# Kernel optimization log

Hardware: AMD Instinct MI355X
Metric: run time of the kernel (lower is better)

The kernel has to match this reference:

```python
import jax, jax.numpy as jnp
import numpy as np

B, IMSIZE, D, L, M, H = 8, 128, 64, 1, 16384, 100
N = B * IMSIZE * IMSIZE


def _build_edges(size, length):
    # build_perception: each pixel connects to all pixels within Chebyshev radius `length`
    ii, jj = np.meshgrid(np.arange(size), np.arange(size), indexing='ij')
    src, dst = [], []
    for dx in range(-length, length + 1):
        for dy in range(-length, length + 1):
            ok = (ii + dx >= 0) & (ii + dx < size) & (jj + dy >= 0) & (jj + dy < size)
            src.append((ii * size + jj)[ok])
            dst.append(((ii + dx) * size + (jj + dy))[ok])
    return np.concatenate(src), np.concatenate(dst)


def setup_inputs() -> dict:
    key = jax.random.key(0)
    ks = jax.random.split(key, 12)
    x = jax.random.normal(ks[0], (N, D), jnp.float32)  # RDN pixel features, flattened
    cluster = jax.random.randint(ks[1], (N,), 0, M).astype(jnp.int32)  # affinity-pool assignment
    s, d = _build_edges(IMSIZE, L)
    offs = (np.arange(B) * IMSIZE * IMSIZE)[:, None]
    edge_src = jnp.asarray((s[None] + offs).reshape(-1), jnp.int32)
    edge_dst = jnp.asarray((d[None] + offs).reshape(-1), jnp.int32)
    ii, jj = np.meshgrid(np.arange(IMSIZE), np.arange(IMSIZE), indexing='ij')
    g = np.stack([ii, jj], -1).reshape(-1, 2).astype(np.float32) / IMSIZE
    coords = jnp.asarray(np.tile(g, (B, 1)))  # spatial_coords.repeat(batch, 1)
    init = lambda k, sh: jax.random.normal(k, sh, jnp.float32) * 0.05
    params = dict(
        W1=init(ks[2], (D + 4, H)), b1=jnp.zeros((H,), jnp.float32),
        W2=init(ks[3], (H, H)), b2=jnp.zeros((H,), jnp.float32),
        W3=init(ks[4], (H, D)), b3=jnp.zeros((D,), jnp.float32),
        Wr=init(ks[5], (D, D)), Wn=init(ks[6], (D, D)), bg=jnp.zeros((D,), jnp.float32),
        Q1w=init(ks[7], (D, H)), Q1b=jnp.zeros((H,), jnp.float32),
        Q2w=init(ks[8], (H, H)), Q2b=jnp.zeros((H,), jnp.float32),
        Q3w=init(ks[9], (H, H)), Q3b=jnp.zeros((H,), jnp.float32),
        Q4w=init(ks[10], (H, 18)), Q4b=jnp.zeros((18,), jnp.float32),
    )
    out = dict(x=x, coords=coords, cluster=cluster, edge_src=edge_src, edge_dst=edge_dst)
    out.update(params)
    return out


def _render_qtr(G, feats):
    # RenderQTR, vectorized over the 3 channels: quadratic texture rendering per pixel
    centers, paras = feats[:, :2], feats[:, 2:20].reshape(-1, 3, 6)
    dx = (G[:, 0] - centers[:, 0])[:, None]
    dy = (G[:, 1] - centers[:, 1])[:, None]
    a, ah, aw, ahh, aww, ahw = (paras[:, :, k] for k in range(6))
    return a + ah * dx + aw * dy + ahh * dx * dx + aww * dy * dy + ahw * dx * dy


def reference(x, coords, cluster, edge_src, edge_dst, W1, b1, W2, b2, W3, b3, Wr, Wn, bg, Q1w, Q1b, Q2w, Q2b, Q3w, Q3b, Q4w, Q4b):
    # --- affinity-aggregation pooling (scatter-mean coarsening) ---
    cnt = jnp.maximum(jax.ops.segment_sum(jnp.ones((N, 1), x.dtype), cluster, num_segments=M), 1.0)
    xp = jax.ops.segment_sum(x, cluster, num_segments=M) / cnt
    cent = jax.ops.segment_sum(coords, cluster, num_segments=M) / cnt          # scatter_mean centroids
    mom = jax.ops.segment_sum(coords * coords, cluster, num_segments=M) / cnt  # scatter_mean moments
    # --- node transform FCBlock on [feat, 10*centroid, 10*moment] ---
    h = jnp.concatenate([xp, 10.0 * cent, 10.0 * mom], axis=-1)
    h = jax.nn.relu(h @ W1 + b1)
    h = jax.nn.relu(h @ W2 + b2)
    h = h @ W3 + b3
    # --- GraphConv(aggr='max') on cluster-coarsened edges (index-chase) ---
    cs, cd = cluster[edge_src], cluster[edge_dst]
    agg = jax.ops.segment_max((h @ Wn)[cs], cd, num_segments=M)
    agg = jnp.where(jnp.isfinite(agg), agg, 0.0)  # empty segments -> 0
    feat = h @ Wr + agg + bg
    # --- node_to_qtr_p2 FCBlock -> joint spatial features ---
    q = jax.nn.relu(feat @ Q1w + Q1b)
    q = jax.nn.relu(q @ Q2w + Q2b)
    q = jax.nn.relu(q @ Q3w + Q3b)
    q = q @ Q4w + Q4b
    jsf = jnp.concatenate([q, cent], axis=-1)[cluster]  # un-pool gather back to pixel nodes
    recon = _render_qtr(coords, jsf)                     # [N, 3]
    return recon.reshape(B, IMSIZE * IMSIZE, 3)          # to_dense_batch (equal-size batches)
```

## Files before the change

### kernel.cpp

```cpp
#include <hip/hip_runtime.h>
#include <hip/hip_fp16.h>
#include <cmath>

#define SSZ    128
#define SS     (SSZ*SSZ)
#define NB     8
#define NNODES (NB*SS)
#define DD     64
#define MM     16384
#define HH     100
#define BINCAP 64
#define KP     136
#define WSLOT  (112*KP)

typedef _Float16 f16x8 __attribute__((ext_vector_type(8)));
typedef _Float16 f16x2 __attribute__((ext_vector_type(2)));
typedef float    f32x4 __attribute__((ext_vector_type(4)));

__device__ __forceinline__ f16x2 hmax2(f16x2 a, f16x2 b) {
    f16x2 r;
    r.x = (a.x > b.x) ? a.x : b.x;
    r.y = (a.y > b.y) ? a.y : b.y;
    return r;
}

__global__ void k_prep(const float* __restrict__ W1, const float* __restrict__ W2,
                       const float* __restrict__ W3, const float* __restrict__ Wn,
                       const float* __restrict__ Wr, const float* __restrict__ Q1w,
                       const float* __restrict__ Q2w, const float* __restrict__ Q3w,
                       const float* __restrict__ Q4w, __half* __restrict__ Wt,
                       int* __restrict__ binCnt) {
    int idx = blockIdx.x * 256 + threadIdx.x;
    if (idx < MM) binCnt[idx] = 0;
    if (idx >= 9 * WSLOT) return;
    int mat = idx / WSLOT, rem = idx - mat * WSLOT;
    int n = rem / KP, k = rem - n * KP;
    const float* src; int K, N;
    switch (mat) {
        case 0: src = W1;  K = 68;  N = 100; break;
        case 1: src = W2;  K = 100; N = 100; break;
        case 2: src = W3;  K = 100; N = 64;  break;
        case 3: src = Wn;  K = 64;  N = 64;  break;
        case 4: src = Wr;  K = 64;  N = 64;  break;
        case 5: src = Q1w; K = 64;  N = 100; break;
        case 6: src = Q2w; K = 100; N = 100; break;
        case 7: src = Q3w; K = 100; N = 100; break;
        default:src = Q4w; K = 100; N = 18;  break;
    }
    float v = (n < N && k < K) ? src[k * N + n] : 0.0f;
    Wt[idx] = __float2half(v);
}

__global__ void k_scatter(const int* __restrict__ cluster,
                          int* __restrict__ binCnt, int* __restrict__ nodeList) {
    int n = blockIdx.x * 256 + threadIdx.x;
    if (n >= NNODES) return;
    int c = cluster[n];
    int pos = atomicAdd(&binCnt[c], 1);
    if (pos < BINCAP) nodeList[c * BINCAP + pos] = n;
}

template<int KC, int NT>
__device__ __forceinline__ void mfma_stage(
    const _Float16* __restrict__ inBuf, _Float16* __restrict__ outBuf,
    const _Float16* __restrict__ Wt, const float* __restrict__ bias,
    int Nout, bool relu, int w, int lane) {
    const int m = lane & 15, q = lane >> 4;
    f16x8 a[KC];
    #pragma unroll
    for (int kc = 0; kc < KC; kc++)
        a[kc] = *(const f16x8*)&inBuf[m * KP + kc * 32 + q * 8];
    #pragma unroll
    for (int tt = 0; tt < (NT + 3) / 4; tt++) {
        const int t = w + tt * 4;
        if (t >= NT) break;
        f32x4 acc = {0.0f, 0.0f, 0.0f, 0.0f};
        #pragma unroll
        for (int kc = 0; kc < KC; kc++) {
            f16x8 b = *(const f16x8*)&Wt[(16 * t + m) * KP + kc * 32 + q * 8];
            acc = __builtin_amdgcn_mfma_f32_16x16x32_f16(a[kc], b, acc, 0, 0, 0);
        }
        const int n = 16 * t + m;
        const float bb = (n < Nout) ? bias[n] : 0.0f;
        #pragma unroll
        for (int r = 0; r < 4; r++) {
            float c = acc[r] + bb;
            if (relu) c = fmaxf(c, 0.0f);
            if (n < Nout) outBuf[(q * 4 + r) * KP + n] = (_Float16)c;
        }
    }
}

__global__ __launch_bounds__(256) void k_mlp1(
    const float* __restrict__ x, const float* __restrict__ coords,
    const int* __restrict__ binCnt, const int* __restrict__ nodeList,
    const __half* __restrict__ WtAll,
    const float* __restrict__ b1, const float* __restrict__ b2,
    const float* __restrict__ b3, const float* __restrict__ bg,
    __half* __restrict__ hWnOut, float* __restrict__ featP,
    float* __restrict__ jsf) {
    __shared__ __align__(16) _Float16 sb0[16 * KP];
    __shared__ __align__(16) _Float16 sb1[16 * KP];
    const _Float16* Wt = (const _Float16*)WtAll;
    const int tid = threadIdx.x, lane = tid & 63, w = tid >> 6;
    const int c0 = blockIdx.x * 16;
    const int m = lane & 15, q = lane >> 4;

    int cnts[4], nls[4];
    #pragma unroll
    for (int cc = 0; cc < 4; cc++) {
        const int c = c0 + w * 4 + cc;
        int ct = binCnt[c];
        cnts[cc] = (ct > BINCAP) ? BINCAP : ct;
        nls[cc]  = nodeList[c * BINCAP + lane];
    }
    float sx[4], sc[4], sm[4];
    #pragma unroll
    for (int cc = 0; cc < 4; cc++) { sx[cc] = 0.0f; sc[cc] = 0.0f; sm[cc] = 0.0f; }

    {
        float v[4][8], cv[4][8];
        #pragma unroll
        for (int cc = 0; cc < 4; cc++) {
            #pragma unroll
            for (int u = 0; u < 8; u++) {
                int n = __shfl(nls[cc], u);
                bool valid = (u < cnts[cc]);
                int ns = valid ? n : 0;
                v[cc][u]  = x[(size_t)ns * 64 + lane];
                cv[cc][u] = (lane < 2) ? coords[ns * 2 + lane] : 0.0f;
                if (!valid) { v[cc][u] = 0.0f; cv[cc][u] = 0.0f; }
            }
        }
        #pragma unroll
        for (int cc = 0; cc < 4; cc++)
            #pragma unroll
            for (int u = 0; u < 8; u++) {
                sx[cc] += v[cc][u];
                sc[cc] += cv[cc][u];
                sm[cc] += cv[cc][u] * cv[cc][u];
            }
    }
    #pragma unroll
    for (int cc = 0; cc < 4; cc++) {
        for (int i0 = 8; i0 < cnts[cc]; i0 += 8) {
            float v[8], cv[8];
            #pragma unroll
            for (int u = 0; u < 8; u++) {
                int i = i0 + u;
                int n = __shfl(nls[cc], i & 63);
                bool valid = (i < cnts[cc]);
                int ns = valid ? n : 0;
                v[u]  = x[(size_t)ns * 64 + lane];
                cv[u] = (lane < 2) ? coords[ns * 2 + lane] : 0.0f;
                if (!valid) { v[u] = 0.0f; cv[u] = 0.0f; }
            }
            #pragma unroll
            for (int u = 0; u < 8; u++) {
                sx[cc] += v[u]; sc[cc] += cv[u]; sm[cc] += cv[u] * cv[u];
            }
        }
    }
    #pragma unroll
    for (int cc = 0; cc < 4; cc++) {
        const int ci = w * 4 + cc;
        const int c  = c0 + ci;
        float fcnt = fmaxf((float)cnts[cc], 1.0f);
        sb0[ci * KP + lane] = (_Float16)(sx[cc] / fcnt);
        if (lane < 2) {
            float cent = sc[cc] / fcnt;
            sb0[ci * KP + 64 + lane] = (_Float16)(10.0f * cent);
            sb0[ci * KP + 66 + lane] = (_Float16)(10.0f * sm[cc] / fcnt);
            jsf[c * 20 + 18 + lane] = cent;
        }
    }
    for (int i = tid; i < 16 * 68; i += 256) {
        int r = i / 68, k = 68 + (i - r * 68);
        sb0[r * KP + k] = (_Float16)0.0f;
    }
    for (int i = tid; i < 16 * 36; i += 256) {
        int r = i / 36, k = 100 + (i - r * 36);
        sb1[r * KP + k] = (_Float16)0.0f;
    }
    __syncthreads();

    mfma_stage<3, 7>(sb0, sb1, Wt + 0 * WSLOT, b1, 100, true,  w, lane);
    __syncthreads();
    mfma_stage<4, 7>(sb1, sb0, Wt + 1 * WSLOT, b2, 100, true,  w, lane);
    __syncthreads();
    mfma_stage<4, 4>(sb0, sb1, Wt + 2 * WSLOT, b3, 64,  false, w, lane);
    __syncthreads();

    {
        const _Float16* Wnt = Wt + 3 * WSLOT;
        const _Float16* Wrt = Wt + 4 * WSLOT;
        f16x8 a0 = *(const f16x8*)&sb1[m * KP + q * 8];
        f16x8 a1 = *(const f16x8*)&sb1[m * KP + 32 + q * 8];
        const int t = w;
        f16x8 bn0 = *(const f16x8*)&Wnt[(16 * t + m) * KP + q * 8];
        f16x8 bn1 = *(const f16x8*)&Wnt[(16 * t + m) * KP + 32 + q * 8];
        f16x8 br0 = *(const f16x8*)&Wrt[(16 * t + m) * KP + q * 8];
        f16x8 br1 = *(const f16x8*)&Wrt[(16 * t + m) * KP + 32 + q * 8];
        f32x4 an = {0.0f, 0.0f, 0.0f, 0.0f};
        f32x4 ar = {0.0f, 0.0f, 0.0f, 0.0f};
        an = __builtin_amdgcn_mfma_f32_16x16x32_f16(a0, bn0, an, 0, 0, 0);
        an = __builtin_amdgcn_mfma_f32_16x16x32_f16(a1, bn1, an, 0, 0, 0);
        ar = __builtin_amdgcn_mfma_f32_16x16x32_f16(a0, br0, ar, 0, 0, 0);
        ar = __builtin_amdgcn_mfma_f32_16x16x32_f16(a1, br1, ar, 0, 0, 0);
        const int n = 16 * t + m;
        const float bgv = bg[n];
        #pragma unroll
        for (int r = 0; r < 4; r++) {
            int row = c0 + q * 4 + r;
            hWnOut[row * 64 + n] = __float2half(an[r]);
            featP [row * 64 + n] = ar[r] + bgv;
        }
    }
}

__global__ __launch_bounds__(512) void k_hvmax(
    const int* __restrict__ cluster, const __half* __restrict__ hWn,
    __half* __restrict__ vmax) {
    __shared__ f16x2 hm[10][16][32];
    const int w = threadIdx.x >> 6, lane = threadIdx.x & 63;
    const int blk  = blockIdx.x;
    const int b    = blk >> 7;
    const int rem  = blk & 127;
    const int r0   = (rem >> 3) << 3;
    const int j0   = (rem & 7) << 4;
    const int base = b * SS;
    const f16x2 NEGH = {(_Float16)-65504.0f, (_Float16)-65504.0f};

    for (int lr = w; lr < 10; lr += 8) {
        int gi = r0 - 1 + lr;
        if (gi < 0 || gi >= SSZ) {
            if (lane < 32) {
                #pragma unroll
                for (int k = 0; k < 16; k++) hm[lr][k][lane] = NEGH;
            }
        } else {
            int rowbase = base + gi * SSZ;
            int jl = j0 - 1 + lane;
            int cid = 0;
            if (lane < 18 && jl >= 0 && jl < SSZ) cid = cluster[rowbase + jl];
            f16x2 val[18];
            #pragma unroll
            for (int p = 0; p < 18; p++) {
                int jp = j0 - 1 + p;
                int cp = __shfl(cid, p);
                val[p] = NEGH;
                if (lane < 32 && jp >= 0 && jp < SSZ)
                    val[p] = *(const f16x2*)&hWn[(cp << 6) + (lane << 1)];
            }
            if (lane < 32) {
                #pragma unroll
                for (int k = 0; k < 16; k++)
                    hm[lr][k][lane] = hmax2(hmax2(val[k], val[k + 1]), val[k + 2]);
            }
        }
    }
    __syncthreads();

    const int outbase = (base + (r0 + w) * SSZ + j0) << 6;
    if (lane < 32) {
        #pragma unroll
        for (int k = 0; k < 16; k++) {
            f16x2 v = hmax2(hmax2(hm[w][k][lane], hm[w + 1][k][lane]),
                            hm[w + 2][k][lane]);
            *(f16x2*)&vmax[outbase + (k << 6) + (lane << 1)] = v;
        }
    }
}

__global__ __launch_bounds__(256) void k_qmlp(
    const float* __restrict__ featP, const __half* __restrict__ vmax,
    const int* __restrict__ binCnt, const int* __restrict__ nodeList,
    const __half* __restrict__ WtAll,
    const float* __restrict__ Q1b, const float* __restrict__ Q2b,
    const float* __restrict__ Q3b, const float* __restrict__ Q4b,
    const float* __restrict__ jsf, const float* __restrict__ coords,
    float* __restrict__ out) {
    __shared__ __align__(16) _Float16 sb0[16 * KP];
    __shared__ __align__(16) _Float16 sb1[16 * KP];
    __shared__ float jsfT[16][20];
    const _Float16* Wt = (const _Float16*)WtAll;
    const int tid = threadIdx.x, lane = tid & 63, w = tid >> 6;
    const int c0 = blockIdx.x * 16;
    const int m = lane & 15, q = lane >> 4;

    int cnts[4], nls[4];
    #pragma unroll
    for (int cc = 0; cc < 4; cc++) {
        const int c = c0 + w * 4 + cc;
        int ct = binCnt[c];
        cnts[cc] = (ct > BINCAP) ? BINCAP : ct;
        nls[cc]  = nodeList[c * BINCAP + lane];
    }
    float mx[4];
    #pragma unroll
    for (int cc = 0; cc < 4; cc++) mx[cc] = -__builtin_inff();

    {
        float v[4][8];
        #pragma unroll
        for (int cc = 0; cc < 4; cc++) {
            #pragma unroll
            for (int u = 0; u < 8; u++) {
                int n = __shfl(nls[cc], u);
                bool valid = (u < cnts[cc]);
                int ns = valid ? n : 0;
                v[cc][u] = __half2float(vmax[((size_t)ns << 6) + lane]);
                if (!valid) v[cc][u] = -__builtin_inff();
            }
        }
        #pragma unroll
        for (int cc = 0; cc < 4; cc++)
            #pragma unroll
            for (int u = 0; u < 8; u++) mx[cc] = fmaxf(mx[cc], v[cc][u]);
    }
    #pragma unroll
    for (int cc = 0; cc < 4; cc++) {
        for (int i0 = 8; i0 < cnts[cc]; i0 += 8) {
            float v[8];
            #pragma unroll
            for (int u = 0; u < 8; u++) {
                int i = i0 + u;
                int n = __shfl(nls[cc], i & 63);
                bool valid = (i < cnts[cc]);
                int ns = valid ? n : 0;
                v[u] = __half2float(vmax[((size_t)ns << 6) + lane]);
                if (!valid) v[u] = -__builtin_inff();
            }
            #pragma unroll
            for (int u = 0; u < 8; u++) mx[cc] = fmaxf(mx[cc], v[u]);
        }
    }
    #pragma unroll
    for (int cc = 0; cc < 4; cc++) {
        const int ci = w * 4 + cc;
        const int c  = c0 + ci;
        float agg = (cnts[cc] == 0) ? 0.0f : mx[cc];
        sb0[ci * KP + lane] = (_Float16)(featP[(size_t)c * 64 + lane] + agg);
    }
    for (int i = tid; i < 16 * 36; i += 256) {
        int r = i / 36, k = 100 + (i - r * 36);
        sb0[r * KP + k] = (_Float16)0.0f;
    }
    for (int i = tid; i < 16 * 36; i += 256) {
        int r = i / 36, k = 100 + (i - r * 36);
        sb1[r * KP + k] = (_Float16)0.0f;
    }
    if (tid < 32)
        jsfT[tid >> 1][18 + (tid & 1)] = jsf[(c0 + (tid >> 1)) * 20 + 18 + (tid & 1)];
    __syncthreads();

    mfma_stage<2, 7>(sb0, sb1, Wt + 5 * WSLOT, Q1b, 100, true, w, lane);
    __syncthreads();
    mfma_stage<4, 7>(sb1, sb0, Wt + 6 * WSLOT, Q2b, 100, true, w, lane);
    __syncthreads();
    mfma_stage<4, 7>(sb0, sb1, Wt + 7 * WSLOT, Q3b, 100, true, w, lane);
    __syncthreads();

    if (w < 2) {
        const _Float16* Q4t = Wt + 8 * WSLOT;
        f16x8 a[4];
        #pragma unroll
        for (int kc = 0; kc < 4; kc++)
            a[kc] = *(const f16x8*)&sb1[m * KP + kc * 32 + q * 8];
        const int t = w;
        f32x4 acc = {0.0f, 0.0f, 0.0f, 0.0f};
        #pragma unroll
        for (int kc = 0; kc < 4; kc++) {
            f16x8 b = *(const f16x8*)&Q4t[(16 * t + m) * KP + kc * 32 + q * 8];
            acc = __builtin_amdgcn_mfma_f32_16x16x32_f16(a[kc], b, acc, 0, 0, 0);
        }
        const int n = 16 * t + m;
        if (n < 18) {
            const float bb = Q4b[n];
            #pragma unroll
            for (int r = 0; r < 4; r++)
                jsfT[q * 4 + r][n] = acc[r] + bb;
        }
    }
    __syncthreads();

    {
        const int ci = tid >> 4;
        const int c  = c0 + ci;
        int cnt = binCnt[c];
        if (cnt > BINCAP) cnt = BINCAP;
        const float* fv = jsfT[ci];
        for (int slot = tid & 15; slot < cnt; slot += 16) {
            int n = nodeList[c * BINCAP + slot];
            float gx = coords[n * 2 + 0], gy = coords[n * 2 + 1];
            float dx = gx - fv[0];
            float dy = gy - fv[1];
            #pragma unroll
            for (int r = 0; r < 3; r++) {
                float a   = fv[2 + r * 6 + 0];
                float ah  = fv[2 + r * 6 + 1];
                float aw  = fv[2 + r * 6 + 2];
                float ahh = fv[2 + r * 6 + 3];
                float aww = fv[2 + r * 6 + 4];
                float ahw = fv[2 + r * 6 + 5];
                out[n * 3 + r] = a + ah * dx + aw * dy + ahh * dx * dx
                               + aww * dy * dy + ahw * dx * dy;
            }
        }
    }
}

extern "C" void kernel_launch(void* const* d_in, const int* in_sizes, int n_in,
                              void* d_out, int out_size, void* d_ws, size_t ws_size,
                              hipStream_t stream) {
    const float* x       = (const float*)d_in[0];
    const float* coords  = (const float*)d_in[1];
    const int*   cluster = (const int*)  d_in[2];
    const float* W1  = (const float*)d_in[5];
    const float* b1  = (const float*)d_in[6];
    const float* W2  = (const float*)d_in[7];
    const float* b2  = (const float*)d_in[8];
    const float* W3  = (const float*)d_in[9];
    const float* b3  = (const float*)d_in[10];
    const float* Wr  = (const float*)d_in[11];
    const float* Wn  = (const float*)d_in[12];
    const float* bg  = (const float*)d_in[13];
    const float* Q1w = (const float*)d_in[14];
    const float* Q1b = (const float*)d_in[15];
    const float* Q2w = (const float*)d_in[16];
    const float* Q2b = (const float*)d_in[17];
    const float* Q3w = (const float*)d_in[18];
    const float* Q3b = (const float*)d_in[19];
    const float* Q4w = (const float*)d_in[20];
    const float* Q4b = (const float*)d_in[21];
    float* out = (float*)d_out;

    int*    binCnt   = (int*)d_ws;
    int*    nodeList = binCnt + MM;
    float*  featP    = (float*)(nodeList + MM * BINCAP);
    float*  jsf      = featP + MM * 64;
    __half* hWnH     = (__half*)(jsf + MM * 20);
    __half* vmaxH    = hWnH + MM * 64;
    __half* WtH      = vmaxH + (size_t)NNODES * 64;

    k_prep   <<<(9 * WSLOT + 255) / 256, 256, 0, stream>>>(W1, W2, W3, Wn, Wr,
                                                           Q1w, Q2w, Q3w, Q4w,
                                                           WtH, binCnt);
    k_scatter<<<(NNODES + 255) / 256, 256, 0, stream>>>(cluster, binCnt, nodeList);
    k_mlp1   <<<MM / 16, 256, 0, stream>>>(x, coords, binCnt, nodeList, WtH,
                                           b1, b2, b3, bg, hWnH, featP, jsf);
    k_hvmax  <<<1024, 512, 0, stream>>>(cluster, hWnH, vmaxH);
    k_qmlp   <<<MM / 16, 256, 0, stream>>>(featP, vmaxH, binCnt, nodeList, WtH,
                                           Q1b, Q2b, Q3b, Q4b, jsf, coords, out);
}
```

Measured before the change: 169.8 us.

## Fuse 3x3 neighbourhood max into qmlp kernel, dropping per-pixel vmax buffer

Removes the k_hvmax kernel, which wrote a per-pixel 3x3-window max of hWn for all 131k pixels. k_qmlp now builds, for each cluster, a shared-memory list of neighbour cluster ids for up to 16 member pixels and gathers hWn rows for them directly, with a slow fallback loop for larger clusters. This cuts a kernel launch and the large fp16 vmax write and read, at the cost of more scattered hWn gathers (9 per member pixel) and extra shared memory and syncs in k_qmlp.

Measured after the change: 185.8 us. 9.4% more time.

```diff
diff --git a/kernel.cpp b/kernel.cpp
--- a/kernel.cpp
+++ b/kernel.cpp
@@ -218,62 +218,9 @@
     }
 }
 
-__global__ __launch_bounds__(512) void k_hvmax(
-    const int* __restrict__ cluster, const __half* __restrict__ hWn,
-    __half* __restrict__ vmax) {
-    __shared__ f16x2 hm[10][16][32];
-    const int w = threadIdx.x >> 6, lane = threadIdx.x & 63;
-    const int blk  = blockIdx.x;
-    const int b    = blk >> 7;
-    const int rem  = blk & 127;
-    const int r0   = (rem >> 3) << 3;
-    const int j0   = (rem & 7) << 4;
-    const int base = b * SS;
-    const f16x2 NEGH = {(_Float16)-65504.0f, (_Float16)-65504.0f};
-
-    for (int lr = w; lr < 10; lr += 8) {
-        int gi = r0 - 1 + lr;
-        if (gi < 0 || gi >= SSZ) {
-            if (lane < 32) {
-                #pragma unroll
-                for (int k = 0; k < 16; k++) hm[lr][k][lane] = NEGH;
-            }
-        } else {
-            int rowbase = base + gi * SSZ;
-            int jl = j0 - 1 + lane;
-            int cid = 0;
-            if (lane < 18 && jl >= 0 && jl < SSZ) cid = cluster[rowbase + jl];
-            f16x2 val[18];
-            #pragma unroll
-            for (int p = 0; p < 18; p++) {
-                int jp = j0 - 1 + p;
-                int cp = __shfl(cid, p);
-                val[p] = NEGH;
-                if (lane < 32 && jp >= 0 && jp < SSZ)
-                    val[p] = *(const f16x2*)&hWn[(cp << 6) + (lane << 1)];
-            }
-            if (lane < 32) {
-                #pragma unroll
-                for (int k = 0; k < 16; k++)
-                    hm[lr][k][lane] = hmax2(hmax2(val[k], val[k + 1]), val[k + 2]);
-            }
-        }
-    }
-    __syncthreads();
-
-    const int outbase = (base + (r0 + w) * SSZ + j0) << 6;
-    if (lane < 32) {
-        #pragma unroll
-        for (int k = 0; k < 16; k++) {
-            f16x2 v = hmax2(hmax2(hm[w][k][lane], hm[w + 1][k][lane]),
-                            hm[w + 2][k][lane]);
-            *(f16x2*)&vmax[outbase + (k << 6) + (lane << 1)] = v;
-        }
-    }
-}
-
 __global__ __launch_bounds__(256) void k_qmlp(
-    const float* __restrict__ featP, const __half* __restrict__ vmax,
+    const float* __restrict__ featP, const __half* __restrict__ hWn,
+    const int* __restrict__ cluster,
     const int* __restrict__ binCnt, const int* __restrict__ nodeList,
     const __half* __restrict__ WtAll,
     const float* __restrict__ Q1b, const float* __restrict__ Q2b,
@@ -283,10 +230,20 @@
     __shared__ __align__(16) _Float16 sb0[16 * KP];
     __shared__ __align__(16) _Float16 sb1[16 * KP];
     __shared__ float jsfT[16][20];
+    __shared__ __align__(16) int cidsL[16][144];
+    __shared__ int cntL[16];
+    __shared__ int nodeL[16][16];
     const _Float16* Wt = (const _Float16*)WtAll;
     const int tid = threadIdx.x, lane = tid & 63, w = tid >> 6;
     const int c0 = blockIdx.x * 16;
     const int m = lane & 15, q = lane >> 4;
+    const int half = lane >> 5, j = lane & 31;
+
+    if (tid < 16) {
+        int ct = binCnt[c0 + tid];
+        cntL[tid] = (ct > BINCAP) ? BINCAP : ct;
+    }
+    nodeL[tid >> 4][tid & 15] = nodeList[(c0 + (tid >> 4)) * BINCAP + (tid & 15)];
 
     int cnts[4], nls[4];
     #pragma unroll
@@ -294,53 +251,24 @@
         const int c = c0 + w * 4 + cc;
         int ct = binCnt[c];
         cnts[cc] = (ct > BINCAP) ? BINCAP : ct;
-        nls[cc]  = nodeList[c * BINCAP + lane];
-    }
-    float mx[4];
-    #pragma unroll
-    for (int cc = 0; cc < 4; cc++) mx[cc] = -__builtin_inff();
-
-    {
-        float v[4][8];
-        #pragma unroll
-        for (int cc = 0; cc < 4; cc++) {
-            #pragma unroll
-            for (int u = 0; u < 8; u++) {
-                int n = __shfl(nls[cc], u);
-                bool valid = (u < cnts[cc]);
-                int ns = valid ? n : 0;
-                v[cc][u] = __half2float(vmax[((size_t)ns << 6) + lane]);
-                if (!valid) v[cc][u] = -__builtin_inff();
-            }
-        }
-        #pragma unroll
-        for (int cc = 0; cc < 4; cc++)
-            #pragma unroll
-            for (int u = 0; u < 8; u++) mx[cc] = fmaxf(mx[cc], v[cc][u]);
-    }
-    #pragma unroll
-    for (int cc = 0; cc < 4; cc++) {
-        for (int i0 = 8; i0 < cnts[cc]; i0 += 8) {
-            float v[8];
-            #pragma unroll
-            for (int u = 0; u < 8; u++) {
-                int i = i0 + u;
-                int n = __shfl(nls[cc], i & 63);
-                bool valid = (i < cnts[cc]);
-                int ns = valid ? n : 0;
-                v[u] = __half2float(vmax[((size_t)ns << 6) + lane]);
-                if (!valid) v[u] = -__builtin_inff();
-            }
-            #pragma unroll
-            for (int u = 0; u < 8; u++) mx[cc] = fmaxf(mx[cc], v[u]);
-        }
-    }
-    #pragma unroll
-    for (int cc = 0; cc < 4; cc++) {
-        const int ci = w * 4 + cc;
-        const int c  = c0 + ci;
-        float agg = (cnts[cc] == 0) ? 0.0f : mx[cc];
-        sb0[ci * KP + lane] = (_Float16)(featP[(size_t)c * 64 + lane] + agg);
+        nls[cc]  = (cnts[cc] > 16) ? nodeList[c * BINCAP + lane] : 0;
+    }
+    __syncthreads();
+
+    for (int i = tid; i < 16 * 144; i += 256) {
+        int ci = i / 144, e = i - ci * 144;
+        int u  = e / 9,   t = e - u * 9;
+        int cid = -1;
+        if (u < cntL[ci]) {
+            int n   = nodeL[ci][u];
+            int pos = n & (SS - 1);
+            int ii  = pos >> 7, jj = pos & 127;
+            int di  = t / 3 - 1, dj = t - (t / 3) * 3 - 1;
+            int ni  = ii + di,   nj = jj + dj;
+            if (ni >= 0 && ni < SSZ && nj >= 0 && nj < SSZ)
+                cid = cluster[n + di * SSZ + dj];
+        }
+        cidsL[ci][e] = cid;
     }
     for (int i = tid; i < 16 * 36; i += 256) {
         int r = i / 36, k = 100 + (i - r * 36);
@@ -352,6 +280,59 @@
     }
     if (tid < 32)
         jsfT[tid >> 1][18 + (tid & 1)] = jsf[(c0 + (tid >> 1)) * 20 + 18 + (tid & 1)];
+    __syncthreads();
+
+    {
+        const f16x2* hWn2 = (const f16x2*)hWn;
+        const f16x2 NEGH = {(_Float16)-65504.0f, (_Float16)-65504.0f};
+        #pragma unroll
+        for (int cc = 0; cc < 4; cc++) {
+            const int ci = w * 4 + cc, c = c0 + ci;
+            const int cnt = cnts[cc];
+            const int cf = (cnt < 16) ? cnt : 16;
+            f16x2 mx = NEGH;
+            const int chunks = (9 * cf + 7) >> 3;
+            for (int k = 0; k < chunks; k++) {
+                const int4* p = (const int4*)&cidsL[ci][k * 8];
+                int4 a = p[0], b4 = p[1];
+                int e0 = half ? a.y  : a.x;
+                int e1 = half ? a.w  : a.z;
+                int e2 = half ? b4.y : b4.x;
+                int e3 = half ? b4.w : b4.z;
+                f16x2 v0 = NEGH, v1 = NEGH, v2 = NEGH, v3 = NEGH;
+                if (e0 >= 0) v0 = hWn2[e0 * 32 + j];
+                if (e1 >= 0) v1 = hWn2[e1 * 32 + j];
+                if (e2 >= 0) v2 = hWn2[e2 * 32 + j];
+                if (e3 >= 0) v3 = hWn2[e3 * 32 + j];
+                mx = hmax2(mx, hmax2(hmax2(v0, v1), hmax2(v2, v3)));
+            }
+            for (int i = 16; i < cnt; i++) {
+                int n   = __shfl(nls[cc], i);
+                int pos = n & (SS - 1);
+                int ii  = pos >> 7, jj = pos & 127;
+                #pragma unroll
+                for (int t = 0; t < 9; t++) {
+                    int di = t / 3 - 1, dj = t - (t / 3) * 3 - 1;
+                    int ni = ii + di, nj = jj + dj;
+                    if (ni >= 0 && ni < SSZ && nj >= 0 && nj < SSZ) {
+                        int cid = cluster[n + di * SSZ + dj];
+                        mx = hmax2(mx, hWn2[cid * 32 + j]);
+                    }
+                }
+            }
+            int xi = __shfl_xor(*(int*)&mx, 32);
+            mx = hmax2(mx, *(f16x2*)&xi);
+            if (lane < 32) {
+                float a0 = 0.0f, a1 = 0.0f;
+                if (cnt != 0) { a0 = (float)mx.x; a1 = (float)mx.y; }
+                const float2 fp = *(const float2*)&featP[(size_t)c * 64 + 2 * j];
+                f16x2 o;
+                o.x = (_Float16)(fp.x + a0);
+                o.y = (_Float16)(fp.y + a1);
+                *(f16x2*)&sb0[ci * KP + 2 * j] = o;
+            }
+        }
+    }
     __syncthreads();
 
     mfma_stage<2, 7>(sb0, sb1, Wt + 5 * WSLOT, Q1b, 100, true, w, lane);
@@ -440,8 +421,7 @@
     float*  featP    = (float*)(nodeList + MM * BINCAP);
     float*  jsf      = featP + MM * 64;
     __half* hWnH     = (__half*)(jsf + MM * 20);
-    __half* vmaxH    = hWnH + MM * 64;
-    __half* WtH      = vmaxH + (size_t)NNODES * 64;
+    __half* WtH      = hWnH + MM * 64;
 
     k_prep   <<<(9 * WSLOT + 255) / 256, 256, 0, stream>>>(W1, W2, W3, Wn, Wr,
                                                            Q1w, Q2w, Q3w, Q4w,
@@ -449,7 +429,6 @@
     k_scatter<<<(NNODES + 255) / 256, 256, 0, stream>>>(cluster, binCnt, nodeList);
     k_mlp1   <<<MM / 16, 256, 0, stream>>>(x, coords, binCnt, nodeList, WtH,
                                            b1, b2, b3, bg, hWnH, featP, jsf);
-    k_hvmax  <<<1024, 512, 0, stream>>>(cluster, hWnH, vmaxH);
-    k_qmlp   <<<MM / 16, 256, 0, stream>>>(featP, vmaxH, binCnt, nodeList, WtH,
-                                           Q1b, Q2b, Q3b, Q4b, jsf, coords, out);
-}
+    k_qmlp   <<<MM / 16, 256, 0, stream>>>(featP, hWnH, cluster, binCnt, nodeList,
+                                           WtH, Q1b, Q2b, Q3b, Q4b, jsf, coords, out);
+}
```

## Write per-pixel window maxima in cluster-binned order for contiguous reduction

Applied to the files above, without the earlier changes.

k_scatter now records each node's slot within its cluster bin. k_hvmax writes each pixel's 3x3 neighbourhood max directly into a cluster-major permuted buffer, so k_qmlp reads each cluster's rows contiguously with 16-byte vector loads and reduces them with a packed f16 max plus cross-lane shuffles. This replaces the earlier per-node gather through nodeList. The cost is scattered writes in k_hvmax, a larger workspace (MM*BINCAP*64 halves), and max accumulation in fp16.

Result: no change. 171.5 us (+1.0%).

```diff
diff --git a/kernel.cpp b/kernel.cpp
--- a/kernel.cpp
+++ b/kernel.cpp
@@ -22,6 +22,21 @@
     r.x = (a.x > b.x) ? a.x : b.x;
     r.y = (a.y > b.y) ? a.y : b.y;
     return r;
+}
+
+__device__ __forceinline__ f16x8 hmax8(f16x8 a, f16x8 b) {
+    f16x8 r;
+    #pragma unroll
+    for (int i = 0; i < 8; i++) r[i] = (a[i] > b[i]) ? a[i] : b[i];
+    return r;
+}
+
+__device__ __forceinline__ f16x8 shfl_xor16B(f16x8 v, int mask) {
+    union { f16x8 h; int i[4]; } u;
+    u.h = v;
+    #pragma unroll
+    for (int t = 0; t < 4; t++) u.i[t] = __shfl_xor(u.i[t], mask);
+    return u.h;
 }
 
 __global__ void k_prep(const float* __restrict__ W1, const float* __restrict__ W2,
@@ -52,12 +67,18 @@
 }
 
 __global__ void k_scatter(const int* __restrict__ cluster,
-                          int* __restrict__ binCnt, int* __restrict__ nodeList) {
+                          int* __restrict__ binCnt, int* __restrict__ nodeList,
+                          int* __restrict__ posOf) {
     int n = blockIdx.x * 256 + threadIdx.x;
     if (n >= NNODES) return;
     int c = cluster[n];
     int pos = atomicAdd(&binCnt[c], 1);
-    if (pos < BINCAP) nodeList[c * BINCAP + pos] = n;
+    if (pos < BINCAP) {
+        nodeList[c * BINCAP + pos] = n;
+        posOf[n] = pos;
+    } else {
+        posOf[n] = BINCAP;
+    }
 }
 
 template<int KC, int NT>
@@ -219,8 +240,8 @@
 }
 
 __global__ __launch_bounds__(512) void k_hvmax(
-    const int* __restrict__ cluster, const __half* __restrict__ hWn,
-    __half* __restrict__ vmax) {
+    const int* __restrict__ cluster, const int* __restrict__ posOf,
+    const __half* __restrict__ hWn, __half* __restrict__ vmaxPerm) {
     __shared__ f16x2 hm[10][16][32];
     const int w = threadIdx.x >> 6, lane = threadIdx.x & 63;
     const int blk  = blockIdx.x;
@@ -231,6 +252,13 @@
     const int base = b * SS;
     const f16x2 NEGH = {(_Float16)-65504.0f, (_Float16)-65504.0f};
 
+    const int p0 = base + (r0 + w) * SSZ + j0;
+    int c2 = 0, pos2 = BINCAP;
+    if (lane < 16) {
+        c2   = cluster[p0 + lane];
+        pos2 = posOf[p0 + lane];
+    }
+
     for (int lr = w; lr < 10; lr += 8) {
         int gi = r0 - 1 + lr;
         if (gi < 0 || gi >= SSZ) {
@@ -261,19 +289,21 @@
     }
     __syncthreads();
 
-    const int outbase = (base + (r0 + w) * SSZ + j0) << 6;
     if (lane < 32) {
         #pragma unroll
         for (int k = 0; k < 16; k++) {
             f16x2 v = hmax2(hmax2(hm[w][k][lane], hm[w + 1][k][lane]),
                             hm[w + 2][k][lane]);
-            *(f16x2*)&vmax[outbase + (k << 6) + (lane << 1)] = v;
+            int cK   = __shfl(c2, k);
+            int posK = __shfl(pos2, k);
+            if (posK < BINCAP)
+                *(f16x2*)&vmaxPerm[((size_t)(cK * BINCAP + posK) << 6) + (lane << 1)] = v;
         }
     }
 }
 
 __global__ __launch_bounds__(256) void k_qmlp(
-    const float* __restrict__ featP, const __half* __restrict__ vmax,
+    const float* __restrict__ featP, const __half* __restrict__ vmaxPerm,
     const int* __restrict__ binCnt, const int* __restrict__ nodeList,
     const __half* __restrict__ WtAll,
     const float* __restrict__ Q1b, const float* __restrict__ Q2b,
@@ -288,59 +318,57 @@
     const int c0 = blockIdx.x * 16;
     const int m = lane & 15, q = lane >> 4;
 
-    int cnts[4], nls[4];
+    int cnts[4];
     #pragma unroll
     for (int cc = 0; cc < 4; cc++) {
-        const int c = c0 + w * 4 + cc;
-        int ct = binCnt[c];
+        int ct = binCnt[c0 + w * 4 + cc];
         cnts[cc] = (ct > BINCAP) ? BINCAP : ct;
-        nls[cc]  = nodeList[c * BINCAP + lane];
-    }
-    float mx[4];
-    #pragma unroll
-    for (int cc = 0; cc < 4; cc++) mx[cc] = -__builtin_inff();
-
+    }
     {
-        float v[4][8];
+        const f16x8 NEG8 = {(_Float16)-65504.0f, (_Float16)-65504.0f,
+                            (_Float16)-65504.0f, (_Float16)-65504.0f,
+                            (_Float16)-65504.0f, (_Float16)-65504.0f,
+                            (_Float16)-65504.0f, (_Float16)-65504.0f};
         #pragma unroll
         for (int cc = 0; cc < 4; cc++) {
-            #pragma unroll
-            for (int u = 0; u < 8; u++) {
-                int n = __shfl(nls[cc], u);
-                bool valid = (u < cnts[cc]);
-                int ns = valid ? n : 0;
-                v[cc][u] = __half2float(vmax[((size_t)ns << 6) + lane]);
-                if (!valid) v[cc][u] = -__builtin_inff();
-            }
-        }
-        #pragma unroll
-        for (int cc = 0; cc < 4; cc++)
-            #pragma unroll
-            for (int u = 0; u < 8; u++) mx[cc] = fmaxf(mx[cc], v[cc][u]);
-    }
-    #pragma unroll
-    for (int cc = 0; cc < 4; cc++) {
-        for (int i0 = 8; i0 < cnts[cc]; i0 += 8) {
-            float v[8];
-            #pragma unroll
-            for (int u = 0; u < 8; u++) {
-                int i = i0 + u;
-                int n = __shfl(nls[cc], i & 63);
-                bool valid = (i < cnts[cc]);
-                int ns = valid ? n : 0;
-                v[u] = __half2float(vmax[((size_t)ns << 6) + lane]);
-                if (!valid) v[u] = -__builtin_inff();
-            }
-            #pragma unroll
-            for (int u = 0; u < 8; u++) mx[cc] = fmaxf(mx[cc], v[u]);
-        }
-    }
-    #pragma unroll
-    for (int cc = 0; cc < 4; cc++) {
-        const int ci = w * 4 + cc;
-        const int c  = c0 + ci;
-        float agg = (cnts[cc] == 0) ? 0.0f : mx[cc];
-        sb0[ci * KP + lane] = (_Float16)(featP[(size_t)c * 64 + lane] + agg);
+            const int ci = w * 4 + cc, c = c0 + ci;
+            const int cnt = cnts[cc];
+            const _Float16* vp = (const _Float16*)vmaxPerm +
+                                 ((size_t)c * BINCAP << 6);
+            f16x8 mx = NEG8;
+            const int batches = (cnt + 7) >> 3;
+            for (int bb = 0; bb < batches; bb++) {
+                int row = (bb << 3) + (lane >> 3);
+                if (row < cnt) {
+                    f16x8 v = *(const f16x8*)&vp[(bb << 9) + lane * 8];
+                    mx = hmax8(mx, v);
+                }
+            }
+            mx = hmax8(mx, shfl_xor16B(mx, 8));
+            mx = hmax8(mx, shfl_xor16B(mx, 16));
+            mx = hmax8(mx, shfl_xor16B(mx, 32));
+            if (lane < 8) {
+                const float4* fp4 = (const float4*)&featP[(size_t)c * 64 + lane * 8];
+                float4 f0 = fp4[0], f1 = fp4[1];
+                f16x8 o;
+                if (cnt == 0) {
+                    o[0] = (_Float16)f0.x; o[1] = (_Float16)f0.y;
+                    o[2] = (_Float16)f0.z; o[3] = (_Float16)f0.w;
+                    o[4] = (_Float16)f1.x; o[5] = (_Float16)f1.y;
+                    o[6] = (_Float16)f1.z; o[7] = (_Float16)f1.w;
+                } else {
+                    o[0] = (_Float16)(f0.x + (float)mx[0]);
+                    o[1] = (_Float16)(f0.y + (float)mx[1]);
+                    o[2] = (_Float16)(f0.z + (float)mx[2]);
+                    o[3] = (_Float16)(f0.w + (float)mx[3]);
+                    o[4] = (_Float16)(f1.x + (float)mx[4]);
+                    o[5] = (_Float16)(f1.y + (float)mx[5]);
+                    o[6] = (_Float16)(f1.z + (float)mx[6]);
+                    o[7] = (_Float16)(f1.w + (float)mx[7]);
+                }
+                *(f16x8*)&sb0[ci * KP + lane * 8] = o;
+            }
+        }
     }
     for (int i = tid; i < 16 * 36; i += 256) {
         int r = i / 36, k = 100 + (i - r * 36);
@@ -437,19 +465,21 @@
 
     int*    binCnt   = (int*)d_ws;
     int*    nodeList = binCnt + MM;
-    float*  featP    = (float*)(nodeList + MM * BINCAP);
+    int*    posOf    = nodeList + MM * BINCAP;
+    float*  featP    = (float*)(posOf + NNODES);
     float*  jsf      = featP + MM * 64;
     __half* hWnH     = (__half*)(jsf + MM * 20);
-    __half* vmaxH    = hWnH + MM * 64;
-    __half* WtH      = vmaxH + (size_t)NNODES * 64;
+    __half* vmaxPerm = hWnH + MM * 64;
+    __half* WtH      = vmaxPerm + (size_t)MM * BINCAP * 64;
 
     k_prep   <<<(9 * WSLOT + 255) / 256, 256, 0, stream>>>(W1, W2, W3, Wn, Wr,
                                                            Q1w, Q2w, Q3w, Q4w,
                                                            WtH, binCnt);
-    k_scatter<<<(NNODES + 255) / 256, 256, 0, stream>>>(cluster, binCnt, nodeList);
+    k_scatter<<<(NNODES + 255) / 256, 256, 0, stream>>>(cluster, binCnt,
+                                                        nodeList, posOf);
     k_mlp1   <<<MM / 16, 256, 0, stream>>>(x, coords, binCnt, nodeList, WtH,
                                            b1, b2, b3, bg, hWnH, featP, jsf);
-    k_hvmax  <<<1024, 512, 0, stream>>>(cluster, hWnH, vmaxH);
-    k_qmlp   <<<MM / 16, 256, 0, stream>>>(featP, vmaxH, binCnt, nodeList, WtH,
-                                           Q1b, Q2b, Q3b, Q4b, jsf, coords, out);
-}
+    k_hvmax  <<<1024, 512, 0, stream>>>(cluster, posOf, hWnH, vmaxPerm);
+    k_qmlp   <<<MM / 16, 256, 0, stream>>>(featP, vmaxPerm, binCnt, nodeList,
+                                           WtH, Q1b, Q2b, Q3b, Q4b, jsf, coords, out);
+}
```
